# Kernel tuning notes

Hardware: AMD Instinct MI355X
Metric: run time of the kernel (lower is better)

## Reference

```python
import jax, jax.numpy as jnp
import numpy as np

N = 50000      # nodes
E = 500000     # edges (before self-loops)
IN = 128       # in_feats
HID = 64       # h_feats (= per-head out channels)
HEADS = 4
G = 16         # number of graphs in batch
OUT = 326000   # out_feats
NEG_SLOPE = 0.2


def setup_inputs() -> dict:
    key = jax.random.key(0)
    ks = jax.random.split(key, 12)
    x = jax.random.normal(ks[0], (N, IN), dtype=jnp.float32)
    edge_index = jax.random.randint(ks[1], (2, E), 0, N, dtype=jnp.int64)
    edge_attr = jax.random.normal(ks[2], (E, 16), dtype=jnp.float32)
    batch = jnp.sort(jax.random.randint(ks[3], (N,), 0, G, dtype=jnp.int64))
    s = 0.05
    W_emb = jax.random.normal(ks[4], (IN, HID), dtype=jnp.float32) * s
    b_emb = jnp.zeros((HID,), dtype=jnp.float32)
    # 3 stacked GATConv layers (hardcoded in the torch module)
    W_gat = jax.random.normal(ks[5], (3, HID, HEADS * HID), dtype=jnp.float32) * s
    att_src = jax.random.normal(ks[6], (3, HEADS, HID), dtype=jnp.float32) * s
    att_dst = jax.random.normal(ks[7], (3, HEADS, HID), dtype=jnp.float32) * s
    b_gat = jnp.zeros((3, HID), dtype=jnp.float32)
    W_fc = jax.random.normal(ks[8], (HID, OUT), dtype=jnp.float32) * s
    b_fc = jnp.zeros((OUT,), dtype=jnp.float32)
    return {"x": x, "edge_index": edge_index, "edge_attr": edge_attr,
            "batch": batch, "W_emb": W_emb, "b_emb": b_emb,
            "W_gat": W_gat, "att_src": att_src, "att_dst": att_dst,
            "b_gat": b_gat, "W_fc": W_fc, "b_fc": b_fc}


def _gat_layer(h, W, a_src, a_dst, b, src, dst):
    # h: [N, HID]; W: [HID, HEADS*HID]; a_*: [HEADS, HID]; b: [HID]
    z = (h @ W).reshape(N, HEADS, HID)                 # [N, H, F]
    al_s = jnp.einsum('nhf,hf->nh', z, a_src)          # [N, H]
    al_d = jnp.einsum('nhf,hf->nh', z, a_dst)          # [N, H]
    e = jax.nn.leaky_relu(al_s[src] + al_d[dst], NEG_SLOPE)  # [E', H]
    # segment softmax over incoming edges of each dst node
    emax = jax.ops.segment_max(e, dst, num_segments=N)
    w = jnp.exp(e - emax[dst])
    denom = jax.ops.segment_sum(w, dst, num_segments=N)
    alpha = w / (denom[dst] + 1e-16)                   # [E', H]
    msg = z[src] * alpha[:, :, None]                   # [E', H, F]
    out = jax.ops.segment_sum(msg, dst, num_segments=N)  # [N, H, F]
    return out.mean(axis=1) + b                        # concat=False -> head mean


def reference(x, edge_index, edge_attr, batch, W_emb, b_emb,
              W_gat, att_src, att_dst, b_gat, W_fc, b_fc):
    # edge_attr is accepted but unused, matching the torch forward.
    loops = jnp.arange(N, dtype=edge_index.dtype)
    src = jnp.concatenate([edge_index[0], loops])      # PyG add_self_loops=True
    dst = jnp.concatenate([edge_index[1], loops])
    h = x @ W_emb + b_emb                              # node embedding
    for l in range(3):
        h = jax.nn.relu(_gat_layer(h, W_gat[l], att_src[l], att_dst[l],
                                   b_gat[l], src, dst))
    # global mean pool over graphs
    sums = jax.ops.segment_sum(h, batch, num_segments=G)
    cnts = jax.ops.segment_sum(jnp.ones((N, 1), h.dtype), batch, num_segments=G)
    hg = sums / jnp.maximum(cnts, 1.0)                 # [G, HID]
    # dropout is identity in eval mode
    return hg @ W_fc + b_fc                            # [G, OUT]
```

## Files before the change

### kernel.cpp

```cpp
#include <hip/hip_runtime.h>
#include <math.h>

#define N_NODES 50000
#define NPAD 50048
#define N_EDGES 500000
#define EP (N_EDGES + N_NODES)
#define IN_F 128
#define HID 64
#define HEADS 4
#define ZD (HEADS * HID)
#define G_B 16
#define OUT_F 326000
#define NEG 0.2f
#define SCAN_BLK 256
#define NBLK_SCAN ((N_NODES + SCAN_BLK - 1) / SCAN_BLK)
#define CAP 64
#define EVS 72
#define NT 64
#define KP 68
#define FC_GS 4
#define FC_NOB ((OUT_F / 4 + 255) / 256)

__global__ void k_init(int* counts, int* cursor, float* pool, float* pool_cnt,
                       const float* __restrict__ W_gat, const float* __restrict__ att_src,
                       const float* __restrict__ att_dst, float* __restrict__ Wstk,
                       float* __restrict__ weff_s, float* __restrict__ weff_d) {
    int idx = blockIdx.x * 256 + threadIdx.x;
    if (idx < N_NODES) { counts[idx] = 1; cursor[idx] = 0; }
    if (idx < G_B * HID) pool[idx] = 0.f;
    if (idx < G_B) pool_cnt[idx] = 0.f;
    if (idx < 3 * ZD * HID) {
        int l = idx / (ZD * HID);
        int rem = idx - l * (ZD * HID);
        int hk = rem >> 6;
        int f = rem & 63;
        int hh = hk >> 6, k = hk & 63;
        Wstk[idx] = 0.25f * W_gat[(size_t)l * HID * ZD + (size_t)k * ZD + hh * HID + f];
    }
    if (idx < 3 * HEADS * HID) {
        int l = idx / (HEADS * HID);
        int rem = idx - l * (HEADS * HID);
        int hh = rem >> 6, i = rem & 63;
        const float* Wl = W_gat + (size_t)l * HID * ZD;
        const float* as = att_src + l * HEADS * HID + hh * HID;
        const float* ad = att_dst + l * HEADS * HID + hh * HID;
        float ss = 0.f, sd = 0.f;
        for (int f = 0; f < HID; f++) {
            float wv = Wl[(size_t)i * ZD + hh * HID + f];
            ss += wv * as[f];
            sd += wv * ad[f];
        }
        weff_s[idx] = ss;
        weff_d[idx] = sd;
    }
}

__global__ void k_count(const int* __restrict__ ei, int* __restrict__ counts) {
    int i = blockIdx.x * 256 + threadIdx.x;
    if (i < N_EDGES) atomicAdd(&counts[ei[N_EDGES + i]], 1);
}

__global__ void k_scan1(const int* __restrict__ counts, int* __restrict__ tmp,
                        int* __restrict__ partial) {
    __shared__ int s[SCAN_BLK];
    int t = threadIdx.x;
    int i = blockIdx.x * SCAN_BLK + t;
    int v = (i < N_NODES) ? counts[i] : 0;
    s[t] = v;
    __syncthreads();
    for (int off = 1; off < SCAN_BLK; off <<= 1) {
        int a = (t >= off) ? s[t - off] : 0;
        __syncthreads();
        s[t] += a;
        __syncthreads();
    }
    if (i < N_NODES) tmp[i] = s[t];
    if (t == SCAN_BLK - 1) partial[blockIdx.x] = s[t];
}

__global__ void k_scan2(int* partial) {
    __shared__ int s[SCAN_BLK];
    int t = threadIdx.x;
    int v = (t < NBLK_SCAN) ? partial[t] : 0;
    s[t] = v;
    __syncthreads();
    for (int off = 1; off < SCAN_BLK; off <<= 1) {
        int a = (t >= off) ? s[t - off] : 0;
        __syncthreads();
        s[t] += a;
        __syncthreads();
    }
    if (t < NBLK_SCAN) partial[t] = s[t] - v;
}

__global__ void k_scan3(const int* __restrict__ tmp, const int* __restrict__ counts,
                        const int* __restrict__ partial, int* __restrict__ offsets) {
    int i = blockIdx.x * 256 + threadIdx.x;
    if (i < N_NODES) offsets[i] = tmp[i] - counts[i] + partial[i >> 8];
    if (i == 0) offsets[N_NODES] = EP;
}

__global__ void k_fill(const int* __restrict__ ei, const int* __restrict__ offsets,
                       int* __restrict__ cursor, int* __restrict__ edge_src) {
    int i = blockIdx.x * 256 + threadIdx.x;
    if (i >= EP) return;
    int s, d;
    if (i < N_EDGES) { s = ei[i]; d = ei[N_EDGES + i]; }
    else             { s = d = i - N_EDGES; }
    int pos = offsets[d] + atomicAdd(&cursor[d], 1);
    edge_src[pos] = s;
}

template<int KDIM, bool RELU, bool ATT>
__global__ __launch_bounds__(256) void k_gemm(const float* __restrict__ A,
                                              const float* __restrict__ B,
                                              const float* __restrict__ bias,
                                              const float* __restrict__ weff_s,
                                              const float* __restrict__ weff_d,
                                              float* __restrict__ hout,
                                              float* __restrict__ al_s,
                                              float* __restrict__ al_d) {
    __shared__ float smem[2 * NT * KP];
    float* aT = smem;
    float* bs = smem + NT * KP;
    int t = threadIdx.x;
    int n0 = blockIdx.x * NT;
    int w = t >> 6, l = t & 63;
    int tn = (w * 4 + (l >> 4)) * 4;
    int tc = (l & 15) * 4;

    float4 a0 = {0,0,0,0}, a1 = {0,0,0,0}, a2 = {0,0,0,0}, a3 = {0,0,0,0};
    for (int kc = 0; kc < KDIM; kc += NT) {
        if (kc) __syncthreads();
        {
            int r = t >> 2, s = t & 3;
            int rg = n0 + r; if (rg >= N_NODES) rg = N_NODES - 1;
            #pragma unroll
            for (int i = 0; i < 4; i++) {
                int q0 = (i * 4 + s) * 4;
                float4 v = *(const float4*)&A[(size_t)rg * KDIM + kc + q0];
                aT[(q0 + 0) * KP + r] = v.x;
                aT[(q0 + 1) * KP + r] = v.y;
                aT[(q0 + 2) * KP + r] = v.z;
                aT[(q0 + 3) * KP + r] = v.w;
            }
        }
        #pragma unroll
        for (int i = 0; i < 4; i++) {
            int idx = i * 256 + t;
            int k = idx >> 4, cq = (idx & 15) * 4;
            *(float4*)&bs[k * KP + cq] = *(const float4*)&B[(size_t)(kc + k) * HID + cq];
        }
        __syncthreads();
        for (int k = 0; k < NT; k++) {
            float4 hn = *(const float4*)&aT[k * KP + tn];
            float4 wc = *(const float4*)&bs[k * KP + tc];
            a0.x += hn.x * wc.x; a0.y += hn.x * wc.y; a0.z += hn.x * wc.z; a0.w += hn.x * wc.w;
            a1.x += hn.y * wc.x; a1.y += hn.y * wc.y; a1.z += hn.y * wc.z; a1.w += hn.y * wc.w;
            a2.x += hn.z * wc.x; a2.y += hn.z * wc.y; a2.z += hn.z * wc.z; a2.w += hn.z * wc.w;
            a3.x += hn.w * wc.x; a3.y += hn.w * wc.y; a3.z += hn.w * wc.z; a3.w += hn.w * wc.w;
        }
    }
    float4 bv = *(const float4*)&bias[tc];
    a0.x += bv.x; a0.y += bv.y; a0.z += bv.z; a0.w += bv.w;
    a1.x += bv.x; a1.y += bv.y; a1.z += bv.z; a1.w += bv.w;
    a2.x += bv.x; a2.y += bv.y; a2.z += bv.z; a2.w += bv.w;
    a3.x += bv.x; a3.y += bv.y; a3.z += bv.z; a3.w += bv.w;
    if (RELU) {
        a0.x = fmaxf(a0.x, 0.f); a0.y = fmaxf(a0.y, 0.f); a0.z = fmaxf(a0.z, 0.f); a0.w = fmaxf(a0.w, 0.f);
        a1.x = fmaxf(a1.x, 0.f); a1.y = fmaxf(a1.y, 0.f); a1.z = fmaxf(a1.z, 0.f); a1.w = fmaxf(a1.w, 0.f);
        a2.x = fmaxf(a2.x, 0.f); a2.y = fmaxf(a2.y, 0.f); a2.z = fmaxf(a2.z, 0.f); a2.w = fmaxf(a2.w, 0.f);
        a3.x = fmaxf(a3.x, 0.f); a3.y = fmaxf(a3.y, 0.f); a3.z = fmaxf(a3.z, 0.f); a3.w = fmaxf(a3.w, 0.f);
    }
    *(float4*)&hout[(size_t)(n0 + tn + 0) * HID + tc] = a0;
    *(float4*)&hout[(size_t)(n0 + tn + 1) * HID + tc] = a1;
    *(float4*)&hout[(size_t)(n0 + tn + 2) * HID + tc] = a2;
    *(float4*)&hout[(size_t)(n0 + tn + 3) * HID + tc] = a3;

    if (ATT) {
        float4 ws4[HEADS], wd4[HEADS];
        #pragma unroll
        for (int hh = 0; hh < HEADS; hh++) {
            ws4[hh] = *(const float4*)&weff_s[hh * HID + tc];
            wd4[hh] = *(const float4*)&weff_d[hh * HID + tc];
        }
        __syncthreads();
        float* pps = smem;
        float* ppd = smem + NT * KP;
        int tcI = l & 15;
        float4 rows[4] = {a0, a1, a2, a3};
        #pragma unroll
        for (int q = 0; q < 4; q++) {
            #pragma unroll
            for (int hh = 0; hh < HEADS; hh++) {
                float ps = rows[q].x * ws4[hh].x + rows[q].y * ws4[hh].y +
                           rows[q].z * ws4[hh].z + rows[q].w * ws4[hh].w;
                float pd = rows[q].x * wd4[hh].x + rows[q].y * wd4[hh].y +
                           rows[q].z * wd4[hh].z + rows[q].w * wd4[hh].w;
                pps[(tn + q) * 68 + hh * 17 + tcI] = ps;
                ppd[(tn + q) * 68 + hh * 17 + tcI] = pd;
            }
        }
        __syncthreads();
        int node = t >> 2, hh = t & 3;
        float s1 = 0.f, s2 = 0.f;
        #pragma unroll
        for (int jj = 0; jj < 16; jj++) {
            s1 += pps[node * 68 + hh * 17 + jj];
            s2 += ppd[node * 68 + hh * 17 + jj];
        }
        al_s[(size_t)(n0 + node) * HEADS + hh] = s1;
        al_d[(size_t)(n0 + node) * HEADS + hh] = s2;
    }
}

__device__ __forceinline__ float lrelu(float v) { return v > 0.f ? v : NEG * v; }

__global__ void k_agg(const int* __restrict__ offsets, const int* __restrict__ edge_src,
                      const float* __restrict__ al_s, const float* __restrict__ al_d,
                      const float* __restrict__ h, float* __restrict__ U) {
    __shared__ float evb[4][HEADS * EVS];
    __shared__ int   sb[4][CAP];
    int t  = threadIdx.x;
    int w  = t >> 6;
    int l  = t & 63;
    int hd = l >> 4;
    int j  = l & 15;
    int d  = blockIdx.x * 4 + w;

    int start = __builtin_amdgcn_readfirstlane(offsets[d]);
    int end   = __builtin_amdgcn_readfirstlane(offsets[d + 1]);
    int deg   = end - start;
    float al_dd = al_d[d * HEADS + hd];

    float m = -INFINITY, ssum = 0.f;
    for (int i = start + j; i < end; i += 16) {
        int s = edge_src[i];
        int slot = i - start;
        if (hd == 0 && slot < CAP) sb[w][slot] = s;
        float ev = lrelu(al_s[s * HEADS + hd] + al_dd);
        if (slot < CAP) evb[w][hd * EVS + slot] = ev;
        float nm = fmaxf(m, ev);
        ssum = ssum * __expf(m - nm) + __expf(ev - nm);
        m = nm;
    }
    float M = m;
    for (int o = 8; o > 0; o >>= 1) M = fmaxf(M, __shfl_xor(M, o));
    float S = ssum * __expf(m - M);
    for (int o = 8; o > 0; o >>= 1) S += __shfl_xor(S, o);
    float inv = 1.f / (S + 1e-16f);
    int stop = deg < CAP ? deg : CAP;
    for (int slot = j; slot < stop; slot += 16)
        evb[w][hd * EVS + slot] = __expf(evb[w][hd * EVS + slot] - M) * inv;

    int hoff = j * 4;
    float4 acc = {0.f, 0.f, 0.f, 0.f};
    if (deg <= CAP) {
        float4 b1 = {0,0,0,0}, b2 = {0,0,0,0}, b3 = {0,0,0,0};
        int slot = 0;
        for (; slot + 8 <= deg; slot += 8) {
            int s0 = sb[w][slot],     s1 = sb[w][slot + 1];
            int s2 = sb[w][slot + 2], s3 = sb[w][slot + 3];
            int s4 = sb[w][slot + 4], s5 = sb[w][slot + 5];
            int s6 = sb[w][slot + 6], s7 = sb[w][slot + 7];
            float w0 = evb[w][hd * EVS + slot];
            float w1 = evb[w][hd * EVS + slot + 1];
            float w2 = evb[w][hd * EVS + slot + 2];
            float w3 = evb[w][hd * EVS + slot + 3];
            float w4 = evb[w][hd * EVS + slot + 4];
            float w5 = evb[w][hd * EVS + slot + 5];
            float w6 = evb[w][hd * EVS + slot + 6];
            float w7 = evb[w][hd * EVS + slot + 7];
            float4 h0 = *(const float4*)&h[(size_t)s0 * HID + hoff];
            float4 h1 = *(const float4*)&h[(size_t)s1 * HID + hoff];
            float4 h2 = *(const float4*)&h[(size_t)s2 * HID + hoff];
            float4 h3 = *(const float4*)&h[(size_t)s3 * HID + hoff];
            float4 h4 = *(const float4*)&h[(size_t)s4 * HID + hoff];
            float4 h5 = *(const float4*)&h[(size_t)s5 * HID + hoff];
            float4 h6 = *(const float4*)&h[(size_t)s6 * HID + hoff];
            float4 h7 = *(const float4*)&h[(size_t)s7 * HID + hoff];
            acc.x += w0 * h0.x; acc.y += w0 * h0.y; acc.z += w0 * h0.z; acc.w += w0 * h0.w;
            b1.x  += w1 * h1.x; b1.y  += w1 * h1.y; b1.z  += w1 * h1.z; b1.w  += w1 * h1.w;
            b2.x  += w2 * h2.x; b2.y  += w2 * h2.y; b2.z  += w2 * h2.z; b2.w  += w2 * h2.w;
            b3.x  += w3 * h3.x; b3.y  += w3 * h3.y; b3.z  += w3 * h3.z; b3.w  += w3 * h3.w;
            acc.x += w4 * h4.x; acc.y += w4 * h4.y; acc.z += w4 * h4.z; acc.w += w4 * h4.w;
            b1.x  += w5 * h5.x; b1.y  += w5 * h5.y; b1.z  += w5 * h5.z; b1.w  += w5 * h5.w;
            b2.x  += w6 * h6.x; b2.y  += w6 * h6.y; b2.z  += w6 * h6.z; b2.w  += w6 * h6.w;
            b3.x  += w7 * h7.x; b3.y  += w7 * h7.y; b3.z  += w7 * h7.z; b3.w  += w7 * h7.w;
        }
        for (; slot + 4 <= deg; slot += 4) {
            int s0 = sb[w][slot],     s1 = sb[w][slot + 1];
            int s2 = sb[w][slot + 2], s3 = sb[w][slot + 3];
            float w0 = evb[w][hd * EVS + slot];
            float w1 = evb[w][hd * EVS + slot + 1];
            float w2 = evb[w][hd * EVS + slot + 2];
            float w3 = evb[w][hd * EVS + slot + 3];
            float4 h0 = *(const float4*)&h[(size_t)s0 * HID + hoff];
            float4 h1 = *(const float4*)&h[(size_t)s1 * HID + hoff];
            float4 h2 = *(const float4*)&h[(size_t)s2 * HID + hoff];
            float4 h3 = *(const float4*)&h[(size_t)s3 * HID + hoff];
            acc.x += w0 * h0.x; acc.y += w0 * h0.y; acc.z += w0 * h0.z; acc.w += w0 * h0.w;
            b1.x  += w1 * h1.x; b1.y  += w1 * h1.y; b1.z  += w1 * h1.z; b1.w  += w1 * h1.w;
            b2.x  += w2 * h2.x; b2.y  += w2 * h2.y; b2.z  += w2 * h2.z; b2.w  += w2 * h2.w;
            b3.x  += w3 * h3.x; b3.y  += w3 * h3.y; b3.z  += w3 * h3.z; b3.w  += w3 * h3.w;
        }
        for (; slot < deg; slot++) {
            int s0 = sb[w][slot];
            float w0 = evb[w][hd * EVS + slot];
            float4 h0 = *(const float4*)&h[(size_t)s0 * HID + hoff];
            acc.x += w0 * h0.x; acc.y += w0 * h0.y; acc.z += w0 * h0.z; acc.w += w0 * h0.w;
        }
        acc.x += b1.x + b2.x + b3.x;
        acc.y += b1.y + b2.y + b3.y;
        acc.z += b1.z + b2.z + b3.z;
        acc.w += b1.w + b2.w + b3.w;
    } else {
        for (int i = start; i < end; i++) {
            int s = __builtin_amdgcn_readfirstlane(edge_src[i]);
            float ev = lrelu(al_s[s * HEADS + hd] + al_dd);
            float alpha = __expf(ev - M) * inv;
            float4 hr = *(const float4*)&h[(size_t)s * HID + hoff];
            acc.x += alpha * hr.x; acc.y += alpha * hr.y;
            acc.z += alpha * hr.z; acc.w += alpha * hr.w;
        }
    }
    *(float4*)&U[(size_t)d * ZD + l * 4] = acc;
}

__global__ __launch_bounds__(256) void k_pool(const float* __restrict__ h,
                                              const int* __restrict__ batch,
                                              float* __restrict__ pool,
                                              float* __restrict__ pool_cnt) {
    int t = threadIdx.x;
    int f  = t & 63;
    int nl = t >> 6;
    int n0 = blockIdx.x * 64 + nl * 16;
    if (n0 >= N_NODES) return;
    int n1 = n0 + 16;
    if (n1 > N_NODES) n1 = N_NODES;
    int curg = batch[n0];
    float acc = 0.f;
    int cnt = 0;
    for (int n = n0; n < n1; n++) {
        int g = batch[n];
        if (g != curg) {
            atomicAdd(&pool[curg * HID + f], acc);
            if (f == 0) atomicAdd(&pool_cnt[curg], (float)cnt);
            acc = 0.f; cnt = 0; curg = g;
        }
        acc += h[(size_t)n * HID + f];
        cnt++;
    }
    atomicAdd(&pool[curg * HID + f], acc);
    if (f == 0) atomicAdd(&pool_cnt[curg], (float)cnt);
}

__global__ __launch_bounds__(256, 1) void k_fc(const float* __restrict__ pool,
                                               const float* __restrict__ pool_cnt,
                                               const float* __restrict__ W_fc,
                                               const float* __restrict__ b_fc,
                                               float* __restrict__ out) {
    __shared__ float hg[FC_GS * HID];
    int t = threadIdx.x;
    int bid = blockIdx.x;
    int bg = (bid >> 3) & (FC_GS - 1);
    int ob = (bid >> 5) * 8 + (bid & 7);
    int g0 = bg * (G_B / FC_GS);
    if (t < FC_GS * HID) {
        int g = g0 + (t >> 6), f = t & 63;
        hg[t] = pool[g * HID + f] / fmaxf(pool_cnt[g], 1.f);
    }
    __syncthreads();
    int o4 = ob * 256 + t;
    if (o4 >= OUT_F / 4) return;
    int o = o4 * 4;
    float4 acc[FC_GS];
    float4 bo = *(const float4*)&b_fc[o];
    #pragma unroll
    for (int g = 0; g < FC_GS; g++) acc[g] = bo;
    for (int kc = 0; kc < HID; kc += 16) {
        float4 wv[16];
        #pragma unroll
        for (int u = 0; u < 16; u++)
            wv[u] = *(const float4*)&W_fc[(size_t)(kc + u) * OUT_F + o];
        #pragma unroll
        for (int u = 0; u < 16; u++) {
            #pragma unroll
            for (int g = 0; g < FC_GS; g++) {
                float hv = hg[g * HID + kc + u];
                acc[g].x += hv * wv[u].x; acc[g].y += hv * wv[u].y;
                acc[g].z += hv * wv[u].z; acc[g].w += hv * wv[u].w;
            }
        }
    }
    #pragma unroll
    for (int g = 0; g < FC_GS; g++)
        *(float4*)&out[(size_t)(g0 + g) * OUT_F + o] = acc[g];
}

extern "C" void kernel_launch(void* const* d_in, const int* in_sizes, int n_in,
                              void* d_out, int out_size, void* d_ws, size_t ws_size,
                              hipStream_t stream) {
    const float* x       = (const float*)d_in[0];
    const int*   ei      = (const int*)d_in[1];
    const int*   batch   = (const int*)d_in[3];
    const float* W_emb   = (const float*)d_in[4];
    const float* b_emb   = (const float*)d_in[5];
    const float* W_gat   = (const float*)d_in[6];
    const float* att_src = (const float*)d_in[7];
    const float* att_dst = (const float*)d_in[8];
    const float* b_gat   = (const float*)d_in[9];
    const float* W_fc    = (const float*)d_in[10];
    const float* b_fc    = (const float*)d_in[11];
    float* out = (float*)d_out;

    char* p = (char*)d_ws;
    auto alloc = [&](size_t bytes) -> void* {
        void* r = (void*)p;
        p += (bytes + 255) & ~(size_t)255;
        return r;
    };
    float* h        = (float*)alloc((size_t)NPAD * HID * 4);
    float* U        = (float*)alloc((size_t)NPAD * ZD * 4);
    float* al_s     = (float*)alloc((size_t)NPAD * HEADS * 4);
    float* al_d     = (float*)alloc((size_t)NPAD * HEADS * 4);
    int*   counts   = (int*)alloc((size_t)N_NODES * 4);
    int*   offsets  = (int*)alloc((size_t)(N_NODES + 1) * 4);
    int*   cursor   = (int*)alloc((size_t)N_NODES * 4);
    int*   tmp      = (int*)alloc((size_t)N_NODES * 4);
    int*   partial  = (int*)alloc((size_t)SCAN_BLK * 4);
    int*   edge_src = (int*)alloc((size_t)EP * 4);
    float* pool     = (float*)alloc((size_t)G_B * HID * 4);
    float* pool_cnt = (float*)alloc((size_t)G_B * 4);
    float* Wstk     = (float*)alloc((size_t)3 * ZD * HID * 4);
    float* weff_s   = (float*)alloc((size_t)3 * HEADS * HID * 4);
    float* weff_d   = (float*)alloc((size_t)3 * HEADS * HID * 4);

    k_init <<<NBLK_SCAN, 256, 0, stream>>>(counts, cursor, pool, pool_cnt,
                                           W_gat, att_src, att_dst,
                                           Wstk, weff_s, weff_d);
    k_count<<<(N_EDGES + 255) / 256, 256, 0, stream>>>(ei, counts);
    k_scan1<<<NBLK_SCAN, SCAN_BLK, 0, stream>>>(counts, tmp, partial);
    k_scan2<<<1, SCAN_BLK, 0, stream>>>(partial);
    k_scan3<<<NBLK_SCAN, 256, 0, stream>>>(tmp, counts, partial, offsets);
    k_fill <<<(EP + 255) / 256, 256, 0, stream>>>(ei, offsets, cursor, edge_src);

    k_gemm<IN_F, false, true><<<NPAD / NT, 256, 0, stream>>>(
        x, W_emb, b_emb, weff_s, weff_d, h, al_s, al_d);

    k_agg<<<N_NODES / 4, 256, 0, stream>>>(offsets, edge_src, al_s, al_d, h, U);
    k_gemm<ZD, true, true><<<NPAD / NT, 256, 0, stream>>>(
        U, Wstk, b_gat, weff_s + ZD, weff_d + ZD, h, al_s, al_d);

    k_agg<<<N_NODES / 4, 256, 0, stream>>>(offsets, edge_src, al_s, al_d, h, U);
    k_gemm<ZD, true, true><<<NPAD / NT, 256, 0, stream>>>(
        U, Wstk + (size_t)ZD * HID, b_gat + HID, weff_s + 2 * ZD, weff_d + 2 * ZD,
        h, al_s, al_d);

    k_agg<<<N_NODES / 4, 256, 0, stream>>>(offsets, edge_src, al_s, al_d, h, U);
    k_gemm<ZD, true, false><<<NPAD / NT, 256, 0, stream>>>(
        U, Wstk + (size_t)2 * ZD * HID, b_gat + 2 * HID, weff_s, weff_d,
        h, al_s, al_d);

    k_pool<<<(N_NODES + 63) / 64, 256, 0, stream>>>(h, batch, pool, pool_cnt);
    k_fc  <<<((FC_NOB + 7) / 8) * 8 * FC_GS, 256, 0, stream>>>(
        pool, pool_cnt, W_fc, b_fc, out);
}
```

Measured before the change: 512.7 us.

## Enlarge GEMM tiles to 256 nodes with 8x8 register blocking and shuffle reductions

Each GEMM block now covers 256 nodes instead of 64 and loads K in chunks of 32. Each thread accumulates an 8x8 register tile, which raises compute per shared-memory load. The attention-logit dot products are now reduced with warp shuffles instead of a shared-memory staging pass, dropping two barriers. The trade-off is a much smaller grid (about 196 blocks on a 256-CU part) with one wave per SIMD, which risks idle CUs and weak latency hiding on what is largely a bandwidth-bound GEMM. Node padding is raised so the grid covers all nodes with 256-row tiles.

```diff
diff --git a/kernel.cpp b/kernel.cpp
--- a/kernel.cpp
+++ b/kernel.cpp
@@ -2,7 +2,7 @@
 #include <math.h>
 
 #define N_NODES 50000
-#define NPAD 50048
+#define NPAD 50176
 #define N_EDGES 500000
 #define EP (N_EDGES + N_NODES)
 #define IN_F 128
@@ -16,8 +16,10 @@
 #define NBLK_SCAN ((N_NODES + SCAN_BLK - 1) / SCAN_BLK)
 #define CAP 64
 #define EVS 72
-#define NT 64
-#define KP 68
+#define GNT 256
+#define KCH 32
+#define AP 260
+#define BP 68
 #define FC_GS 4
 #define FC_NOB ((OUT_F / 4 + 255) / 256)
 
@@ -112,105 +114,109 @@
 }
 
 template<int KDIM, bool RELU, bool ATT>
-__global__ __launch_bounds__(256) void k_gemm(const float* __restrict__ A,
-                                              const float* __restrict__ B,
-                                              const float* __restrict__ bias,
-                                              const float* __restrict__ weff_s,
-                                              const float* __restrict__ weff_d,
-                                              float* __restrict__ hout,
-                                              float* __restrict__ al_s,
-                                              float* __restrict__ al_d) {
-    __shared__ float smem[2 * NT * KP];
-    float* aT = smem;
-    float* bs = smem + NT * KP;
+__global__ __launch_bounds__(256, 1) void k_gemm(const float* __restrict__ A,
+                                                 const float* __restrict__ B,
+                                                 const float* __restrict__ bias,
+                                                 const float* __restrict__ weff_s,
+                                                 const float* __restrict__ weff_d,
+                                                 float* __restrict__ hout,
+                                                 float* __restrict__ al_s,
+                                                 float* __restrict__ al_d) {
+    __shared__ float aT[KCH * AP];
+    __shared__ float bs[KCH * BP];
     int t = threadIdx.x;
-    int n0 = blockIdx.x * NT;
-    int w = t >> 6, l = t & 63;
-    int tn = (w * 4 + (l >> 4)) * 4;
-    int tc = (l & 15) * 4;
-
-    float4 a0 = {0,0,0,0}, a1 = {0,0,0,0}, a2 = {0,0,0,0}, a3 = {0,0,0,0};
-    for (int kc = 0; kc < KDIM; kc += NT) {
+    int n0 = blockIdx.x * GNT;
+    int ng = t >> 3;
+    int cg = t & 7;
+
+    float4 acc[8][2];
+    #pragma unroll
+    for (int i = 0; i < 8; i++) {
+        acc[i][0] = make_float4(0.f, 0.f, 0.f, 0.f);
+        acc[i][1] = make_float4(0.f, 0.f, 0.f, 0.f);
+    }
+
+    for (int kc = 0; kc < KDIM; kc += KCH) {
         if (kc) __syncthreads();
-        {
-            int r = t >> 2, s = t & 3;
-            int rg = n0 + r; if (rg >= N_NODES) rg = N_NODES - 1;
-            #pragma unroll
-            for (int i = 0; i < 4; i++) {
-                int q0 = (i * 4 + s) * 4;
-                float4 v = *(const float4*)&A[(size_t)rg * KDIM + kc + q0];
-                aT[(q0 + 0) * KP + r] = v.x;
-                aT[(q0 + 1) * KP + r] = v.y;
-                aT[(q0 + 2) * KP + r] = v.z;
-                aT[(q0 + 3) * KP + r] = v.w;
-            }
-        }
         #pragma unroll
-        for (int i = 0; i < 4; i++) {
+        for (int i = 0; i < 8; i++) {
+            int fid = i * 256 + t;
+            int row = fid >> 3, f4 = (fid & 7) * 4;
+            int rg = n0 + row; if (rg >= N_NODES) rg = N_NODES - 1;
+            float4 v = *(const float4*)&A[(size_t)rg * KDIM + kc + f4];
+            aT[(f4 + 0) * AP + row] = v.x;
+            aT[(f4 + 1) * AP + row] = v.y;
+            aT[(f4 + 2) * AP + row] = v.z;
+            aT[(f4 + 3) * AP + row] = v.w;
+        }
+        #pragma unroll
+        for (int i = 0; i < 2; i++) {
             int idx = i * 256 + t;
             int k = idx >> 4, cq = (idx & 15) * 4;
-            *(float4*)&bs[k * KP + cq] = *(const float4*)&B[(size_t)(kc + k) * HID + cq];
+            *(float4*)&bs[k * BP + cq] = *(const float4*)&B[(size_t)(kc + k) * HID + cq];
         }
         __syncthreads();
-        for (int k = 0; k < NT; k++) {
-            float4 hn = *(const float4*)&aT[k * KP + tn];
-            float4 wc = *(const float4*)&bs[k * KP + tc];
-            a0.x += hn.x * wc.x; a0.y += hn.x * wc.y; a0.z += hn.x * wc.z; a0.w += hn.x * wc.w;
-            a1.x += hn.y * wc.x; a1.y += hn.y * wc.y; a1.z += hn.y * wc.z; a1.w += hn.y * wc.w;
-            a2.x += hn.z * wc.x; a2.y += hn.z * wc.y; a2.z += hn.z * wc.z; a2.w += hn.z * wc.w;
-            a3.x += hn.w * wc.x; a3.y += hn.w * wc.y; a3.z += hn.w * wc.z; a3.w += hn.w * wc.w;
-        }
-    }
-    float4 bv = *(const float4*)&bias[tc];
-    a0.x += bv.x; a0.y += bv.y; a0.z += bv.z; a0.w += bv.w;
-    a1.x += bv.x; a1.y += bv.y; a1.z += bv.z; a1.w += bv.w;
-    a2.x += bv.x; a2.y += bv.y; a2.z += bv.z; a2.w += bv.w;
-    a3.x += bv.x; a3.y += bv.y; a3.z += bv.z; a3.w += bv.w;
-    if (RELU) {
-        a0.x = fmaxf(a0.x, 0.f); a0.y = fmaxf(a0.y, 0.f); a0.z = fmaxf(a0.z, 0.f); a0.w = fmaxf(a0.w, 0.f);
-        a1.x = fmaxf(a1.x, 0.f); a1.y = fmaxf(a1.y, 0.f); a1.z = fmaxf(a1.z, 0.f); a1.w = fmaxf(a1.w, 0.f);
-        a2.x = fmaxf(a2.x, 0.f); a2.y = fmaxf(a2.y, 0.f); a2.z = fmaxf(a2.z, 0.f); a2.w = fmaxf(a2.w, 0.f);
-        a3.x = fmaxf(a3.x, 0.f); a3.y = fmaxf(a3.y, 0.f); a3.z = fmaxf(a3.z, 0.f); a3.w = fmaxf(a3.w, 0.f);
-    }
-    *(float4*)&hout[(size_t)(n0 + tn + 0) * HID + tc] = a0;
-    *(float4*)&hout[(size_t)(n0 + tn + 1) * HID + tc] = a1;
-    *(float4*)&hout[(size_t)(n0 + tn + 2) * HID + tc] = a2;
-    *(float4*)&hout[(size_t)(n0 + tn + 3) * HID + tc] = a3;
+        #pragma unroll 4
+        for (int k = 0; k < KCH; k++) {
+            float4 a0 = *(const float4*)&aT[k * AP + ng * 8];
+            float4 a1 = *(const float4*)&aT[k * AP + ng * 8 + 4];
+            float4 b0 = *(const float4*)&bs[k * BP + cg * 8];
+            float4 b1 = *(const float4*)&bs[k * BP + cg * 8 + 4];
+            float av[8] = {a0.x, a0.y, a0.z, a0.w, a1.x, a1.y, a1.z, a1.w};
+            #pragma unroll
+            for (int i = 0; i < 8; i++) {
+                float a = av[i];
+                acc[i][0].x += a * b0.x; acc[i][0].y += a * b0.y;
+                acc[i][0].z += a * b0.z; acc[i][0].w += a * b0.w;
+                acc[i][1].x += a * b1.x; acc[i][1].y += a * b1.y;
+                acc[i][1].z += a * b1.z; acc[i][1].w += a * b1.w;
+            }
+        }
+    }
+
+    float4 bo0 = *(const float4*)&bias[cg * 8];
+    float4 bo1 = *(const float4*)&bias[cg * 8 + 4];
+    #pragma unroll
+    for (int i = 0; i < 8; i++) {
+        acc[i][0].x += bo0.x; acc[i][0].y += bo0.y; acc[i][0].z += bo0.z; acc[i][0].w += bo0.w;
+        acc[i][1].x += bo1.x; acc[i][1].y += bo1.y; acc[i][1].z += bo1.z; acc[i][1].w += bo1.w;
+        if (RELU) {
+            acc[i][0].x = fmaxf(acc[i][0].x, 0.f); acc[i][0].y = fmaxf(acc[i][0].y, 0.f);
+            acc[i][0].z = fmaxf(acc[i][0].z, 0.f); acc[i][0].w = fmaxf(acc[i][0].w, 0.f);
+            acc[i][1].x = fmaxf(acc[i][1].x, 0.f); acc[i][1].y = fmaxf(acc[i][1].y, 0.f);
+            acc[i][1].z = fmaxf(acc[i][1].z, 0.f); acc[i][1].w = fmaxf(acc[i][1].w, 0.f);
+        }
+        size_t n = (size_t)(n0 + ng * 8 + i);
+        *(float4*)&hout[n * HID + cg * 8]     = acc[i][0];
+        *(float4*)&hout[n * HID + cg * 8 + 4] = acc[i][1];
+    }
 
     if (ATT) {
-        float4 ws4[HEADS], wd4[HEADS];
         #pragma unroll
         for (int hh = 0; hh < HEADS; hh++) {
-            ws4[hh] = *(const float4*)&weff_s[hh * HID + tc];
-            wd4[hh] = *(const float4*)&weff_d[hh * HID + tc];
-        }
-        __syncthreads();
-        float* pps = smem;
-        float* ppd = smem + NT * KP;
-        int tcI = l & 15;
-        float4 rows[4] = {a0, a1, a2, a3};
-        #pragma unroll
-        for (int q = 0; q < 4; q++) {
+            float4 ws0 = *(const float4*)&weff_s[hh * HID + cg * 8];
+            float4 ws1 = *(const float4*)&weff_s[hh * HID + cg * 8 + 4];
+            float4 wd0 = *(const float4*)&weff_d[hh * HID + cg * 8];
+            float4 wd1 = *(const float4*)&weff_d[hh * HID + cg * 8 + 4];
             #pragma unroll
-            for (int hh = 0; hh < HEADS; hh++) {
-                float ps = rows[q].x * ws4[hh].x + rows[q].y * ws4[hh].y +
-                           rows[q].z * ws4[hh].z + rows[q].w * ws4[hh].w;
-                float pd = rows[q].x * wd4[hh].x + rows[q].y * wd4[hh].y +
-                           rows[q].z * wd4[hh].z + rows[q].w * wd4[hh].w;
-                pps[(tn + q) * 68 + hh * 17 + tcI] = ps;
-                ppd[(tn + q) * 68 + hh * 17 + tcI] = pd;
+            for (int i = 0; i < 8; i++) {
+                float ps = acc[i][0].x * ws0.x + acc[i][0].y * ws0.y +
+                           acc[i][0].z * ws0.z + acc[i][0].w * ws0.w +
+                           acc[i][1].x * ws1.x + acc[i][1].y * ws1.y +
+                           acc[i][1].z * ws1.z + acc[i][1].w * ws1.w;
+                float pd = acc[i][0].x * wd0.x + acc[i][0].y * wd0.y +
+                           acc[i][0].z * wd0.z + acc[i][0].w * wd0.w +
+                           acc[i][1].x * wd1.x + acc[i][1].y * wd1.y +
+                           acc[i][1].z * wd1.z + acc[i][1].w * wd1.w;
+                ps += __shfl_xor(ps, 1); ps += __shfl_xor(ps, 2); ps += __shfl_xor(ps, 4);
+                pd += __shfl_xor(pd, 1); pd += __shfl_xor(pd, 2); pd += __shfl_xor(pd, 4);
+                if (cg == hh) {
+                    size_t n = (size_t)(n0 + ng * 8 + i);
+                    al_s[n * HEADS + hh] = ps;
+                    al_d[n * HEADS + hh] = pd;
+                }
             }
         }
-        __syncthreads();
-        int node = t >> 2, hh = t & 3;
-        float s1 = 0.f, s2 = 0.f;
-        #pragma unroll
-        for (int jj = 0; jj < 16; jj++) {
-            s1 += pps[node * 68 + hh * 17 + jj];
-            s2 += ppd[node * 68 + hh * 17 + jj];
-        }
-        al_s[(size_t)(n0 + node) * HEADS + hh] = s1;
-        al_d[(size_t)(n0 + node) * HEADS + hh] = s2;
     }
 }
 
@@ -445,20 +451,20 @@
     k_scan3<<<NBLK_SCAN, 256, 0, stream>>>(tmp, counts, partial, offsets);
     k_fill <<<(EP + 255) / 256, 256, 0, stream>>>(ei, offsets, cursor, edge_src);
 
-    k_gemm<IN_F, false, true><<<NPAD / NT, 256, 0, stream>>>(
+    k_gemm<IN_F, false, true><<<NPAD / GNT, 256, 0, stream>>>(
         x, W_emb, b_emb, weff_s, weff_d, h, al_s, al_d);
 
     k_agg<<<N_NODES / 4, 256, 0, stream>>>(offsets, edge_src, al_s, al_d, h, U);
-    k_gemm<ZD, true, true><<<NPAD / NT, 256, 0, stream>>>(
+    k_gemm<ZD, true, true><<<NPAD / GNT, 256, 0, stream>>>(
         U, Wstk, b_gat, weff_s + ZD, weff_d + ZD, h, al_s, al_d);
 
     k_agg<<<N_NODES / 4, 256, 0, stream>>>(offsets, edge_src, al_s, al_d, h, U);
-    k_gemm<ZD, true, true><<<NPAD / NT, 256, 0, stream>>>(
+    k_gemm<ZD, true, true><<<NPAD / GNT, 256, 0, stream>>>(
         U, Wstk + (size_t)ZD * HID, b_gat + HID, weff_s + 2 * ZD, weff_d + 2 * ZD,
         h, al_s, al_d);
 
     k_agg<<<N_NODES / 4, 256, 0, stream>>>(offsets, edge_src, al_s, al_d, h, U);
-    k_gemm<ZD, true, false><<<NPAD / NT, 256, 0, stream>>>(
+    k_gemm<ZD, true, false><<<NPAD / GNT, 256, 0, stream>>>(
         U, Wstk + (size_t)2 * ZD * HID, b_gat + 2 * HID, weff_s, weff_d,
         h, al_s, al_d);
 
```

Measured after the change: 569.4 us. +11.1%, slower.
